# Kernel optimization log

Measured on AMD Instinct MI355X. Metric: run time of the kernel, lower is better.

## Reference

```python
import jax, jax.numpy as jnp
import numpy as np

M = 8      # window size
S = 4      # shift size
NH = 3     # num heads
EPS = 1e-5


def _rel_pos_index(m):
    coords = np.stack(np.meshgrid(np.arange(m), np.arange(m), indexing='ij')).reshape(2, -1)
    rel = (coords[:, :, None] - coords[:, None, :]).transpose(1, 2, 0)
    rel[:, :, 0] += m - 1
    rel[:, :, 1] += m - 1
    rel[:, :, 0] *= 2 * m - 1
    return rel.sum(-1)  # [m^2, m^2]


def _attn_mask(Hs, Ws, m, s):
    img = np.zeros((Hs, Ws))
    cnt = 0
    for hsl in (slice(0, -m), slice(-m, -s), slice(-s, None)):
        for wsl in (slice(0, -m), slice(-m, -s), slice(-s, None)):
            img[hsl, wsl] = cnt
            cnt += 1
    mw = img.reshape(Hs // m, m, Ws // m, m).transpose(0, 2, 1, 3).reshape(-1, m * m)
    d = mw[:, None, :] - mw[:, :, None]
    return np.where(d != 0, -100.0, 0.0).astype(np.float32)  # [nW, N, N]


def _ln(x, w, b):
    mu = jnp.mean(x, -1, keepdims=True)
    var = jnp.mean(jnp.square(x - mu), -1, keepdims=True)
    return (x - mu) * jax.lax.rsqrt(var + EPS) * w + b


def setup_inputs() -> dict:
    key = jax.random.key(0)
    ks = jax.random.split(key, 8)
    B, Hs, Ws, C = 16, 128, 128, 96
    MLPH = 4 * C
    inp = {
        'x': jax.random.normal(ks[0], (B, Hs * Ws, C), jnp.float32),
        'norm1_w': jnp.ones((C,), jnp.float32),
        'norm1_b': jnp.zeros((C,), jnp.float32),
        'qkv_w': jax.random.normal(ks[1], (C, 3 * C), jnp.float32) * 0.02,
        'qkv_b': jnp.zeros((3 * C,), jnp.float32),
        'rpb_table': jax.random.normal(ks[2], ((2 * M - 1) ** 2, NH), jnp.float32) * 0.02,
        'proj_w': jax.random.normal(ks[3], (C, C), jnp.float32) * 0.02,
        'proj_b': jnp.zeros((C,), jnp.float32),
        'norm2_w': jnp.ones((C,), jnp.float32),
        'norm2_b': jnp.zeros((C,), jnp.float32),
        'mlp_w1': jax.random.normal(ks[4], (C, MLPH), jnp.float32) * 0.02,
        'mlp_b1': jnp.zeros((MLPH,), jnp.float32),
        'mlp_w2': jax.random.normal(ks[5], (MLPH, C), jnp.float32) * 0.02,
        'mlp_b2': jnp.zeros((C,), jnp.float32),
        'H': Hs,
        'W': Ws,
    }
    return inp


def reference(x, norm1_w, norm1_b, qkv_w, qkv_b, rpb_table, proj_w, proj_b,
              norm2_w, norm2_b, mlp_w1, mlp_b1, mlp_w2, mlp_b2, H, W):
    B, L, C = x.shape
    N = M * M
    HD = C // NH
    scale = HD ** -0.5
    nW = (H // M) * (W // M)

    rpi = jnp.asarray(_rel_pos_index(M))                    # [N, N]
    mask = jnp.asarray(_attn_mask(H, W, M, S))              # [nW, N, N]

    shortcut = x
    h = _ln(x, norm1_w, norm1_b).reshape(B, H, W, C)
    h = jnp.roll(h, (-S, -S), axis=(1, 2))
    # window partition -> [B, nW, N, C]
    h = h.reshape(B, H // M, M, W // M, M, C).transpose(0, 1, 3, 2, 4, 5)
    h = h.reshape(B, nW, N, C)

    qkv = (h @ qkv_w + qkv_b).reshape(B, nW, N, 3, NH, HD)
    q, k, v = qkv[..., 0, :, :], qkv[..., 1, :, :], qkv[..., 2, :, :]  # [B,nW,N,NH,HD]
    attn = jnp.einsum('bwnhd,bwmhd->bwhnm', q, k) * scale              # [B,nW,NH,N,N]
    rp_bias = rpb_table[rpi].transpose(2, 0, 1)                        # [NH,N,N]
    attn = attn + rp_bias[None, None] + mask[None, :, None]
    attn = jax.nn.softmax(attn, axis=-1)
    out = jnp.einsum('bwhnm,bwmhd->bwnhd', attn, v).reshape(B, nW, N, C)
    out = out @ proj_w + proj_b

    # window reverse -> [B, H, W, C]
    out = out.reshape(B, H // M, W // M, M, M, C).transpose(0, 1, 3, 2, 4, 5)
    out = out.reshape(B, H, W, C)
    out = jnp.roll(out, (S, S), axis=(1, 2)).reshape(B, L, C)

    x1 = shortcut + out
    h2 = _ln(x1, norm2_w, norm2_b)
    h2 = jax.nn.gelu(h2 @ mlp_w1 + mlp_b1, approximate=False) @ mlp_w2 + mlp_b2
    return x1 + h2
```

## Files before the change

kernel.cpp:

```cpp
#include <hip/hip_runtime.h>
#include <hip/hip_bf16.h>

typedef __hip_bfloat16 hbf16;
typedef __bf16 bf16_t;
typedef __bf16 bf16x8 __attribute__((ext_vector_type(8)));
typedef float  f32x4  __attribute__((ext_vector_type(4)));

__device__ __forceinline__ float b2f(hbf16 v) { return __bfloat162float(v); }

__device__ __forceinline__ float ldx(const void* p, size_t i, bool f32) {
    return f32 ? ((const float*)p)[i] : b2f(((const hbf16*)p)[i]);
}

constexpr int Hh  = 128, Ww = 128, Cc = 96;
constexpr int MM  = 8, SS = 4, NHh = 3, C3 = 288;
constexpr int MLPH = 384;
constexpr int NWH = Hh / MM;
constexpr int NW  = NWH * NWH;
constexpr float SCALE = 0.17677669529663687f;
constexpr float EPSf  = 1e-5f;

constexpr int WQKV_ELEMS = C3 * Cc;
constexpr int WP_ELEMS   = Cc * Cc;
constexpr int W1_ELEMS   = MLPH * Cc;
constexpr int W2_ELEMS   = Cc * MLPH;
constexpr int W_TOTAL    = WQKV_ELEMS + WP_ELEMS + W1_ELEMS + W2_ELEMS;

constexpr int OFF_HA  = 0;
constexpr int OFF_QO  = 6144;
constexpr int OFF_KA  = 12288;
constexpr int OFF_VT  = 18432;
constexpr int OFF_HID = 12288;
constexpr int SMEM_E  = 24576;

__global__ void prep_w(const void* __restrict__ qkvw, const void* __restrict__ pw,
                       const void* __restrict__ w1,   const void* __restrict__ w2,
                       const void* __restrict__ n1w,  bf16_t* __restrict__ ws)
{
    const bool f32 = (((const unsigned*)n1w)[0] == 0x3F800000u);
    int i = blockIdx.x * 256 + threadIdx.x;
    if (i < WQKV_ELEMS) {
        int j = i / Cc, k = i - j * Cc;
        ws[i] = (bf16_t)ldx(qkvw, (size_t)k * C3 + j, f32);
    } else if (i < WQKV_ELEMS + WP_ELEMS) {
        int t = i - WQKV_ELEMS;
        int j = t / Cc, k = t - j * Cc;
        ws[i] = (bf16_t)ldx(pw, (size_t)k * Cc + j, f32);
    } else if (i < WQKV_ELEMS + WP_ELEMS + W1_ELEMS) {
        int t = i - WQKV_ELEMS - WP_ELEMS;
        int j = t / Cc, k = t - j * Cc;
        ws[i] = (bf16_t)ldx(w1, (size_t)k * MLPH + j, f32);
    } else if (i < W_TOTAL) {
        int t = i - WQKV_ELEMS - WP_ELEMS - W1_ELEMS;
        int n = t / MLPH, k = t - n * MLPH;
        ws[i] = (bf16_t)ldx(w2, (size_t)k * Cc + n, f32);
    }
}

__global__ __launch_bounds__(256, 3)
void swin_fused(const void* __restrict__ x,
                const void* __restrict__ n1w, const void* __restrict__ n1b,
                const void* __restrict__ qkvb, const void* __restrict__ rpb,
                const void* __restrict__ pb,
                const void* __restrict__ n2w, const void* __restrict__ n2b,
                const void* __restrict__ b1,  const void* __restrict__ b2,
                const bf16_t* __restrict__ wq_t, const bf16_t* __restrict__ wp_t,
                const bf16_t* __restrict__ w1_t, const bf16_t* __restrict__ w2_t,
                float* __restrict__ out)
{
    __shared__ __align__(16) bf16_t sm[SMEM_E];
    const bool f32 = (((const unsigned*)n1w)[0] == 0x3F800000u);

    const int tid  = threadIdx.x;
    const int lane = tid & 63;
    const int wv   = tid >> 6;
    const int c16  = lane & 15;
    const int quad = lane >> 4;
    const int b    = blockIdx.x / NW;
    const int w    = blockIdx.x % NW;
    const int wi   = w / NWH, wj = w % NWH;

    {
        const int t = tid >> 2, q = tid & 3;
        const int ri = wi * MM + (t >> 3), rj = wj * MM + (t & 7);
        const int gi = (ri + SS) & (Hh - 1), gj = (rj + SS) & (Ww - 1);
        const size_t base = ((size_t)((b * Hh + gi) * Ww + gj)) * Cc + q * 24;
        float v[24]; float s = 0.f, s2 = 0.f;
        if (f32) {
            const float* xf = (const float*)x + base;
            #pragma unroll
            for (int i = 0; i < 6; ++i) {
                float4 t4 = *(const float4*)(xf + i * 4);
                v[i*4+0] = t4.x; v[i*4+1] = t4.y; v[i*4+2] = t4.z; v[i*4+3] = t4.w;
            }
        } else {
            #pragma unroll
            for (int i = 0; i < 24; ++i) v[i] = b2f(((const hbf16*)x)[base + i]);
        }
        #pragma unroll
        for (int i = 0; i < 24; ++i) { s += v[i]; s2 += v[i] * v[i]; }
        s  += __shfl_xor(s, 1);  s  += __shfl_xor(s, 2);
        s2 += __shfl_xor(s2, 1); s2 += __shfl_xor(s2, 2);
        const float mu = s / Cc, var = s2 / Cc - mu * mu, rstd = rsqrtf(var + EPSf);
        #pragma unroll
        for (int ch = 0; ch < 3; ++ch) {
            bf16x8 pk;
            #pragma unroll
            for (int i = 0; i < 8; ++i) {
                int cidx = q * 24 + ch * 8 + i;
                pk[i] = (bf16_t)((v[ch * 8 + i] - mu) * rstd * ldx(n1w, cidx, f32) + ldx(n1b, cidx, f32));
            }
            *(bf16x8*)&sm[OFF_HA + ((q * 3 + ch) * 64 + t) * 8] = pk;
        }
    }

    {
        bf16x8 ha[3];
        #pragma unroll
        for (int ks = 0; ks < 3; ++ks)
            ha[ks] = *(const bf16x8*)&sm[OFF_HA + ((ks * 4 + quad) * 64 + wv * 16 + c16) * 8];
        for (int nt = 0; nt < 18; ++nt) {
            const int j = nt * 16 + c16;
            const bf16_t* wrow = wq_t + (size_t)j * Cc + quad * 8;
            bf16x8 b0 = *(const bf16x8*)(wrow);
            bf16x8 b1v = *(const bf16x8*)(wrow + 32);
            bf16x8 b2v = *(const bf16x8*)(wrow + 64);
            f32x4 acc = {0.f, 0.f, 0.f, 0.f};
            acc = __builtin_amdgcn_mfma_f32_16x16x32_bf16(ha[0], b0, acc, 0, 0, 0);
            acc = __builtin_amdgcn_mfma_f32_16x16x32_bf16(ha[1], b1v, acc, 0, 0, 0);
            acc = __builtin_amdgcn_mfma_f32_16x16x32_bf16(ha[2], b2v, acc, 0, 0, 0);
            const float bias = ldx(qkvb, j, f32);
            #pragma unroll
            for (int r = 0; r < 4; ++r) {
                const int m = wv * 16 + quad * 4 + r;
                const bf16_t vb = (bf16_t)(acc[r] + bias);
                if (j < 96) {
                    int hd = j >> 5, d = j & 31;
                    sm[OFF_QO + ((hd * 4 + (d >> 3)) * 64 + m) * 8 + (d & 7)] = vb;
                } else if (j < 192) {
                    int jj = j - 96; int hd = jj >> 5, d = jj & 31;
                    sm[OFF_KA + ((hd * 4 + (d >> 3)) * 64 + m) * 8 + (d & 7)] = vb;
                } else {
                    int jj = j - 192; int hd = jj >> 5, d = jj & 31;
                    sm[OFF_VT + ((hd * 8 + (m >> 3)) * 32 + d) * 8 + (m & 7)] = vb;
                }
            }
        }
    }
    __syncthreads();

    int regq[4];
    #pragma unroll
    for (int r = 0; r < 4; ++r) {
        int qt = wv * 16 + quad * 4 + r;
        int rq = wi * MM + (qt >> 3), cq = wj * MM + (qt & 7);
        regq[r] = (rq < Hh - MM ? 0 : (rq < Hh - SS ? 1 : 2)) * 3
                + (cq < Ww - MM ? 0 : (cq < Ww - SS ? 1 : 2));
    }

    for (int hd = 0; hd < NHh; ++hd) {
        bf16x8 qa = *(const bf16x8*)&sm[OFF_QO + ((hd * 4 + quad) * 64 + wv * 16 + c16) * 8];
        f32x4 sacc[4];
        #pragma unroll
        for (int nt = 0; nt < 4; ++nt) {
            bf16x8 kb = *(const bf16x8*)&sm[OFF_KA + ((hd * 4 + quad) * 64 + nt * 16 + c16) * 8];
            f32x4 z = {0.f, 0.f, 0.f, 0.f};
            sacc[nt] = __builtin_amdgcn_mfma_f32_16x16x32_bf16(qa, kb, z, 0, 0, 0);
        }
        #pragma unroll
        for (int nt = 0; nt < 4; ++nt) {
            const int kt = nt * 16 + c16;
            const int ki = kt >> 3, kj = kt & 7;
            const int rk = wi * MM + ki, ck = wj * MM + kj;
            const int regk = (rk < Hh - MM ? 0 : (rk < Hh - SS ? 1 : 2)) * 3
                           + (ck < Ww - MM ? 0 : (ck < Ww - SS ? 1 : 2));
            #pragma unroll
            for (int r = 0; r < 4; ++r) {
                const int qt = wv * 16 + quad * 4 + r;
                const int qi = qt >> 3, qj = qt & 7;
                const int rpi = (qi - ki + 7) * 15 + (qj - kj + 7);
                float sv = sacc[nt][r] * SCALE + ldx(rpb, (size_t)rpi * NHh + hd, f32);
                if (regq[r] != regk) sv -= 100.0f;
                sacc[nt][r] = sv;
            }
        }
        float inv[4];
        #pragma unroll
        for (int r = 0; r < 4; ++r) {
            float mx = fmaxf(fmaxf(sacc[0][r], sacc[1][r]), fmaxf(sacc[2][r], sacc[3][r]));
            mx = fmaxf(mx, __shfl_xor(mx, 1)); mx = fmaxf(mx, __shfl_xor(mx, 2));
            mx = fmaxf(mx, __shfl_xor(mx, 4)); mx = fmaxf(mx, __shfl_xor(mx, 8));
            float s = 0.f;
            #pragma unroll
            for (int nt = 0; nt < 4; ++nt) { sacc[nt][r] = __expf(sacc[nt][r] - mx); s += sacc[nt][r]; }
            s += __shfl_xor(s, 1); s += __shfl_xor(s, 2);
            s += __shfl_xor(s, 4); s += __shfl_xor(s, 8);
            inv[r] = 1.0f / s;
        }
        #pragma unroll
        for (int nt = 0; nt < 4; ++nt) {
            const int kt = nt * 16 + c16;
            #pragma unroll
            for (int r = 0; r < 4; ++r) {
                const int qt = wv * 16 + quad * 4 + r;
                sm[OFF_HA + ((kt >> 3) * 64 + qt) * 8 + (kt & 7)] = (bf16_t)(sacc[nt][r] * inv[r]);
            }
        }
        #pragma unroll
        for (int nt2 = 0; nt2 < 2; ++nt2) {
            f32x4 acc = {0.f, 0.f, 0.f, 0.f};
            #pragma unroll
            for (int ks = 0; ks < 2; ++ks) {
                bf16x8 pa = *(const bf16x8*)&sm[OFF_HA + ((ks * 4 + quad) * 64 + wv * 16 + c16) * 8];
                bf16x8 vb = *(const bf16x8*)&sm[OFF_VT + ((hd * 8 + ks * 4 + quad) * 32 + nt2 * 16 + c16) * 8];
                acc = __builtin_amdgcn_mfma_f32_16x16x32_bf16(pa, vb, acc, 0, 0, 0);
            }
            const int chan = hd * 32 + nt2 * 16 + c16;
            #pragma unroll
            for (int r = 0; r < 4; ++r) {
                const int m = wv * 16 + quad * 4 + r;
                sm[OFF_QO + ((chan >> 3) * 64 + m) * 8 + (chan & 7)] = (bf16_t)acc[r];
            }
        }
    }

    int gbase[4];
    #pragma unroll
    for (int r = 0; r < 4; ++r) {
        const int m = wv * 16 + quad * 4 + r;
        const int ri = wi * MM + (m >> 3), rj = wj * MM + (m & 7);
        const int gi = (ri + SS) & (Hh - 1), gj = (rj + SS) & (Ww - 1);
        gbase[r] = ((b * Hh + gi) * Ww + gj) * Cc;
    }

    float x1r[24];
    {
        bf16x8 oa[3];
        #pragma unroll
        for (int ks = 0; ks < 3; ++ks)
            oa[ks] = *(const bf16x8*)&sm[OFF_QO + ((ks * 4 + quad) * 64 + wv * 16 + c16) * 8];
        #pragma unroll
        for (int nt = 0; nt < 6; ++nt) {
            const int n = nt * 16 + c16;
            const bf16_t* wrow = wp_t + (size_t)n * Cc + quad * 8;
            f32x4 acc = {0.f, 0.f, 0.f, 0.f};
            acc = __builtin_amdgcn_mfma_f32_16x16x32_bf16(oa[0], *(const bf16x8*)(wrow),      acc, 0, 0, 0);
            acc = __builtin_amdgcn_mfma_f32_16x16x32_bf16(oa[1], *(const bf16x8*)(wrow + 32), acc, 0, 0, 0);
            acc = __builtin_amdgcn_mfma_f32_16x16x32_bf16(oa[2], *(const bf16x8*)(wrow + 64), acc, 0, 0, 0);
            const float bias = ldx(pb, n, f32);
            #pragma unroll
            for (int r = 0; r < 4; ++r)
                x1r[nt * 4 + r] = ldx(x, (size_t)(gbase[r] + n), f32) + acc[r] + bias;
        }
    }

    float mu_[4], rs_[4];
    #pragma unroll
    for (int r = 0; r < 4; ++r) {
        float s = 0.f, s2 = 0.f;
        #pragma unroll
        for (int nt = 0; nt < 6; ++nt) { float v = x1r[nt * 4 + r]; s += v; s2 += v * v; }
        s  += __shfl_xor(s, 1);  s  += __shfl_xor(s, 2);  s  += __shfl_xor(s, 4);  s  += __shfl_xor(s, 8);
        s2 += __shfl_xor(s2, 1); s2 += __shfl_xor(s2, 2); s2 += __shfl_xor(s2, 4); s2 += __shfl_xor(s2, 8);
        float mu = s / Cc, var = s2 / Cc - mu * mu;
        mu_[r] = mu; rs_[r] = rsqrtf(var + EPSf);
    }
    #pragma unroll
    for (int nt = 0; nt < 6; ++nt) {
        const int c = nt * 16 + c16;
        const float wc = ldx(n2w, c, f32), bc = ldx(n2b, c, f32);
        #pragma unroll
        for (int r = 0; r < 4; ++r) {
            const int m = wv * 16 + quad * 4 + r;
            sm[OFF_QO + ((c >> 3) * 64 + m) * 8 + (c & 7)] =
                (bf16_t)((x1r[nt * 4 + r] - mu_[r]) * rs_[r] * wc + bc);
        }
    }
    __syncthreads();

    {
        bf16x8 h2a[3];
        #pragma unroll
        for (int ks = 0; ks < 3; ++ks)
            h2a[ks] = *(const bf16x8*)&sm[OFF_QO + ((ks * 4 + quad) * 64 + wv * 16 + c16) * 8];

        f32x4 acc2[6];
        #pragma unroll
        for (int nt2 = 0; nt2 < 6; ++nt2) acc2[nt2] = {0.f, 0.f, 0.f, 0.f};

        #pragma unroll
        for (int ck = 0; ck < 2; ++ck) {
            for (int nt = 0; nt < 12; ++nt) {
                const int jl = nt * 16 + c16;
                const int j  = ck * 192 + jl;
                const bf16_t* wrow = w1_t + (size_t)j * Cc + quad * 8;
                f32x4 acc = {0.f, 0.f, 0.f, 0.f};
                acc = __builtin_amdgcn_mfma_f32_16x16x32_bf16(h2a[0], *(const bf16x8*)(wrow),      acc, 0, 0, 0);
                acc = __builtin_amdgcn_mfma_f32_16x16x32_bf16(h2a[1], *(const bf16x8*)(wrow + 32), acc, 0, 0, 0);
                acc = __builtin_amdgcn_mfma_f32_16x16x32_bf16(h2a[2], *(const bf16x8*)(wrow + 64), acc, 0, 0, 0);
                const float bj = ldx(b1, j, f32);
                #pragma unroll
                for (int r = 0; r < 4; ++r) {
                    float a = acc[r] + bj;
                    float y = 1.5957691216f * a * (1.0f + 0.044715f * a * a);
                    float g = a / (1.0f + __expf(-y));
                    const int m = wv * 16 + quad * 4 + r;
                    sm[OFF_HID + ((jl >> 3) * 64 + m) * 8 + (jl & 7)] = (bf16_t)g;
                }
            }
            bf16x8 ha2[6];
            #pragma unroll
            for (int ks = 0; ks < 6; ++ks)
                ha2[ks] = *(const bf16x8*)&sm[OFF_HID + ((ks * 4 + quad) * 64 + wv * 16 + c16) * 8];
            #pragma unroll
            for (int nt2 = 0; nt2 < 6; ++nt2) {
                const int n = nt2 * 16 + c16;
                const bf16_t* wrow = w2_t + (size_t)n * MLPH + ck * 192 + quad * 8;
                #pragma unroll
                for (int ks = 0; ks < 6; ++ks)
                    acc2[nt2] = __builtin_amdgcn_mfma_f32_16x16x32_bf16(ha2[ks], *(const bf16x8*)(wrow + ks * 32), acc2[nt2], 0, 0, 0);
            }
        }

        #pragma unroll
        for (int nt2 = 0; nt2 < 6; ++nt2) {
            const int n = nt2 * 16 + c16;
            const float bn = ldx(b2, n, f32);
            #pragma unroll
            for (int r = 0; r < 4; ++r)
                out[gbase[r] + n] = x1r[nt2 * 4 + r] + acc2[nt2][r] + bn;
        }
    }
}

extern "C" void kernel_launch(void* const* d_in, const int* in_sizes, int n_in,
                              void* d_out, int out_size, void* d_ws, size_t ws_size,
                              hipStream_t stream)
{
    const void* x    = d_in[0];
    const void* n1w  = d_in[1];
    const void* n1b  = d_in[2];
    const void* qkvw = d_in[3];
    const void* qkvb = d_in[4];
    const void* rpb  = d_in[5];
    const void* pw   = d_in[6];
    const void* pb   = d_in[7];
    const void* n2w  = d_in[8];
    const void* n2b  = d_in[9];
    const void* w1   = d_in[10];
    const void* b1   = d_in[11];
    const void* w2   = d_in[12];
    const void* b2   = d_in[13];

    const int B = in_sizes[0] / (Hh * Ww * Cc);
    float* out = (float*)d_out;
    bf16_t* wq_t = (bf16_t*)d_ws;
    bf16_t* wp_t = wq_t + WQKV_ELEMS;
    bf16_t* w1_t = wp_t + WP_ELEMS;
    bf16_t* w2_t = w1_t + W1_ELEMS;

    prep_w<<<(W_TOTAL + 255) / 256, 256, 0, stream>>>(qkvw, pw, w1, w2, n1w, wq_t);

    swin_fused<<<B * NW, 256, 0, stream>>>(x, n1w, n1b, qkvb, rpb, pb,
                                           n2w, n2b, b1, b2,
                                           wq_t, wp_t, w1_t, w2_t, out);
}
```

Baseline: 533.4 us.

## Compute transposed attention scores to keep softmax probabilities in registers

```diff
diff --git a/kernel.cpp b/kernel.cpp
--- a/kernel.cpp
+++ b/kernel.cpp
@@ -3,6 +3,7 @@
 
 typedef __hip_bfloat16 hbf16;
 typedef __bf16 bf16_t;
+typedef __bf16 bf16x4 __attribute__((ext_vector_type(4)));
 typedef __bf16 bf16x8 __attribute__((ext_vector_type(8)));
 typedef float  f32x4  __attribute__((ext_vector_type(4)));
 
@@ -26,12 +27,11 @@
 constexpr int W2_ELEMS   = Cc * MLPH;
 constexpr int W_TOTAL    = WQKV_ELEMS + WP_ELEMS + W1_ELEMS + W2_ELEMS;
 
-constexpr int OFF_HA  = 0;
-constexpr int OFF_QO  = 6144;
-constexpr int OFF_KA  = 12288;
-constexpr int OFF_VT  = 18432;
-constexpr int OFF_HID = 12288;
-constexpr int SMEM_E  = 24576;
+constexpr int OFF_A   = 0;
+constexpr int OFF_KA  = 6144;
+constexpr int OFF_VT  = 12288;
+constexpr int OFF_HID = 6144;
+constexpr int SMEM_E  = 18432;
 
 __global__ void prep_w(const void* __restrict__ qkvw, const void* __restrict__ pw,
                        const void* __restrict__ w1,   const void* __restrict__ w2,
@@ -57,7 +57,7 @@
     }
 }
 
-__global__ __launch_bounds__(256, 3)
+__global__ __launch_bounds__(256, 4)
 void swin_fused(const void* __restrict__ x,
                 const void* __restrict__ n1w, const void* __restrict__ n1b,
                 const void* __restrict__ qkvb, const void* __restrict__ rpb,
@@ -110,7 +110,7 @@
                 int cidx = q * 24 + ch * 8 + i;
                 pk[i] = (bf16_t)((v[ch * 8 + i] - mu) * rstd * ldx(n1w, cidx, f32) + ldx(n1b, cidx, f32));
             }
-            *(bf16x8*)&sm[OFF_HA + ((q * 3 + ch) * 64 + t) * 8] = pk;
+            *(bf16x8*)&sm[OFF_A + ((q * 3 + ch) * 64 + t) * 8] = pk;
         }
     }
 
@@ -118,7 +118,7 @@
         bf16x8 ha[3];
         #pragma unroll
         for (int ks = 0; ks < 3; ++ks)
-            ha[ks] = *(const bf16x8*)&sm[OFF_HA + ((ks * 4 + quad) * 64 + wv * 16 + c16) * 8];
+            ha[ks] = *(const bf16x8*)&sm[OFF_A + ((ks * 4 + quad) * 64 + wv * 16 + c16) * 8];
         for (int nt = 0; nt < 18; ++nt) {
             const int j = nt * 16 + c16;
             const bf16_t* wrow = wq_t + (size_t)j * Cc + quad * 8;
@@ -136,7 +136,7 @@
                 const bf16_t vb = (bf16_t)(acc[r] + bias);
                 if (j < 96) {
                     int hd = j >> 5, d = j & 31;
-                    sm[OFF_QO + ((hd * 4 + (d >> 3)) * 64 + m) * 8 + (d & 7)] = vb;
+                    sm[OFF_A + ((hd * 4 + (d >> 3)) * 64 + m) * 8 + (d & 7)] = vb;
                 } else if (j < 192) {
                     int jj = j - 96; int hd = jj >> 5, d = jj & 31;
                     sm[OFF_KA + ((hd * 4 + (d >> 3)) * 64 + m) * 8 + (d & 7)] = vb;
@@ -149,77 +149,93 @@
     }
     __syncthreads();
 
-    int regq[4];
-    #pragma unroll
-    for (int r = 0; r < 4; ++r) {
-        int qt = wv * 16 + quad * 4 + r;
-        int rq = wi * MM + (qt >> 3), cq = wj * MM + (qt & 7);
-        regq[r] = (rq < Hh - MM ? 0 : (rq < Hh - SS ? 1 : 2)) * 3
-                + (cq < Ww - MM ? 0 : (cq < Ww - SS ? 1 : 2));
-    }
-
-    for (int hd = 0; hd < NHh; ++hd) {
-        bf16x8 qa = *(const bf16x8*)&sm[OFF_QO + ((hd * 4 + quad) * 64 + wv * 16 + c16) * 8];
-        f32x4 sacc[4];
-        #pragma unroll
-        for (int nt = 0; nt < 4; ++nt) {
-            bf16x8 kb = *(const bf16x8*)&sm[OFF_KA + ((hd * 4 + quad) * 64 + nt * 16 + c16) * 8];
-            f32x4 z = {0.f, 0.f, 0.f, 0.f};
-            sacc[nt] = __builtin_amdgcn_mfma_f32_16x16x32_bf16(qa, kb, z, 0, 0, 0);
-        }
-        #pragma unroll
-        for (int nt = 0; nt < 4; ++nt) {
-            const int kt = nt * 16 + c16;
-            const int ki = kt >> 3, kj = kt & 7;
-            const int rk = wi * MM + ki, ck = wj * MM + kj;
-            const int regk = (rk < Hh - MM ? 0 : (rk < Hh - SS ? 1 : 2)) * 3
-                           + (ck < Ww - MM ? 0 : (ck < Ww - SS ? 1 : 2));
+    const int qt_tok = wv * 16 + c16;
+    const int qi = qt_tok >> 3, qj = qt_tok & 7;
+    {
+        const int rq = wi * MM + qi, cq = wj * MM + qj;
+        const int regq = (rq < Hh - MM ? 0 : (rq < Hh - SS ? 1 : 2)) * 3
+                       + (cq < Ww - MM ? 0 : (cq < Ww - SS ? 1 : 2));
+        int   rpi16[16];
+        float pen16[16];
+        #pragma unroll
+        for (int nt = 0; nt < 4; ++nt)
             #pragma unroll
             for (int r = 0; r < 4; ++r) {
-                const int qt = wv * 16 + quad * 4 + r;
-                const int qi = qt >> 3, qj = qt & 7;
-                const int rpi = (qi - ki + 7) * 15 + (qj - kj + 7);
-                float sv = sacc[nt][r] * SCALE + ldx(rpb, (size_t)rpi * NHh + hd, f32);
-                if (regq[r] != regk) sv -= 100.0f;
-                sacc[nt][r] = sv;
-            }
-        }
-        float inv[4];
-        #pragma unroll
-        for (int r = 0; r < 4; ++r) {
-            float mx = fmaxf(fmaxf(sacc[0][r], sacc[1][r]), fmaxf(sacc[2][r], sacc[3][r]));
-            mx = fmaxf(mx, __shfl_xor(mx, 1)); mx = fmaxf(mx, __shfl_xor(mx, 2));
-            mx = fmaxf(mx, __shfl_xor(mx, 4)); mx = fmaxf(mx, __shfl_xor(mx, 8));
+                const int k = nt * 16 + quad * 4 + r;
+                const int ki = k >> 3, kj = k & 7;
+                const int rk = wi * MM + ki, ck = wj * MM + kj;
+                const int regk = (rk < Hh - MM ? 0 : (rk < Hh - SS ? 1 : 2)) * 3
+                               + (ck < Ww - MM ? 0 : (ck < Ww - SS ? 1 : 2));
+                rpi16[nt * 4 + r] = ((qi - ki + 7) * 15 + (qj - kj + 7)) * NHh;
+                pen16[nt * 4 + r] = (regq != regk) ? -100.0f : 0.0f;
+            }
+
+        for (int hd = 0; hd < NHh; ++hd) {
+            bf16x8 qa = *(const bf16x8*)&sm[OFF_A + ((hd * 4 + quad) * 64 + qt_tok) * 8];
+            f32x4 sacc[4];
+            #pragma unroll
+            for (int nt = 0; nt < 4; ++nt) {
+                bf16x8 kb = *(const bf16x8*)&sm[OFF_KA + ((hd * 4 + quad) * 64 + nt * 16 + c16) * 8];
+                f32x4 z = {0.f, 0.f, 0.f, 0.f};
+                sacc[nt] = __builtin_amdgcn_mfma_f32_16x16x32_bf16(kb, qa, z, 0, 0, 0);
+            }
+            #pragma unroll
+            for (int nt = 0; nt < 4; ++nt)
+                #pragma unroll
+                for (int r = 0; r < 4; ++r)
+                    sacc[nt][r] = sacc[nt][r] * SCALE
+                                + ldx(rpb, (size_t)(rpi16[nt * 4 + r] + hd), f32)
+                                + pen16[nt * 4 + r];
+            f32x4 m4 = sacc[0];
+            #pragma unroll
+            for (int nt = 1; nt < 4; ++nt)
+                #pragma unroll
+                for (int r = 0; r < 4; ++r) m4[r] = fmaxf(m4[r], sacc[nt][r]);
+            float mx = fmaxf(fmaxf(m4[0], m4[1]), fmaxf(m4[2], m4[3]));
+            mx = fmaxf(mx, __shfl_xor(mx, 16));
+            mx = fmaxf(mx, __shfl_xor(mx, 32));
             float s = 0.f;
             #pragma unroll
-            for (int nt = 0; nt < 4; ++nt) { sacc[nt][r] = __expf(sacc[nt][r] - mx); s += sacc[nt][r]; }
-            s += __shfl_xor(s, 1); s += __shfl_xor(s, 2);
-            s += __shfl_xor(s, 4); s += __shfl_xor(s, 8);
-            inv[r] = 1.0f / s;
-        }
-        #pragma unroll
-        for (int nt = 0; nt < 4; ++nt) {
-            const int kt = nt * 16 + c16;
+            for (int nt = 0; nt < 4; ++nt)
+                #pragma unroll
+                for (int r = 0; r < 4; ++r) {
+                    float e = __expf(sacc[nt][r] - mx);
+                    sacc[nt][r] = e; s += e;
+                }
+            s += __shfl_xor(s, 16);
+            s += __shfl_xor(s, 32);
+            const float inv = 1.0f / s;
+            bf16x8 pb01, pb23;
             #pragma unroll
             for (int r = 0; r < 4; ++r) {
-                const int qt = wv * 16 + quad * 4 + r;
-                sm[OFF_HA + ((kt >> 3) * 64 + qt) * 8 + (kt & 7)] = (bf16_t)(sacc[nt][r] * inv[r]);
-            }
-        }
-        #pragma unroll
-        for (int nt2 = 0; nt2 < 2; ++nt2) {
-            f32x4 acc = {0.f, 0.f, 0.f, 0.f};
-            #pragma unroll
-            for (int ks = 0; ks < 2; ++ks) {
-                bf16x8 pa = *(const bf16x8*)&sm[OFF_HA + ((ks * 4 + quad) * 64 + wv * 16 + c16) * 8];
-                bf16x8 vb = *(const bf16x8*)&sm[OFF_VT + ((hd * 8 + ks * 4 + quad) * 32 + nt2 * 16 + c16) * 8];
-                acc = __builtin_amdgcn_mfma_f32_16x16x32_bf16(pa, vb, acc, 0, 0, 0);
-            }
-            const int chan = hd * 32 + nt2 * 16 + c16;
-            #pragma unroll
-            for (int r = 0; r < 4; ++r) {
-                const int m = wv * 16 + quad * 4 + r;
-                sm[OFF_QO + ((chan >> 3) * 64 + m) * 8 + (chan & 7)] = (bf16_t)acc[r];
+                pb01[r]     = (bf16_t)(sacc[0][r] * inv);
+                pb01[4 + r] = (bf16_t)(sacc[1][r] * inv);
+                pb23[r]     = (bf16_t)(sacc[2][r] * inv);
+                pb23[4 + r] = (bf16_t)(sacc[3][r] * inv);
+            }
+            const int g2 = quad >> 1, o2 = (quad & 1) * 4;
+            #pragma unroll
+            for (int ct = 0; ct < 2; ++ct) {
+                const int d = ct * 16 + c16;
+                const int vb0 = OFF_VT + ((hd * 8 + g2) * 32 + d) * 8 + o2;
+                bf16x4 v0 = *(const bf16x4*)&sm[vb0];
+                bf16x4 v1 = *(const bf16x4*)&sm[vb0 + 512];
+                bf16x4 v2 = *(const bf16x4*)&sm[vb0 + 1024];
+                bf16x4 v3 = *(const bf16x4*)&sm[vb0 + 1536];
+                bf16x8 va01, va23;
+                #pragma unroll
+                for (int i = 0; i < 4; ++i) {
+                    va01[i] = v0[i]; va01[4 + i] = v1[i];
+                    va23[i] = v2[i]; va23[4 + i] = v3[i];
+                }
+                f32x4 acc = {0.f, 0.f, 0.f, 0.f};
+                acc = __builtin_amdgcn_mfma_f32_16x16x32_bf16(va01, pb01, acc, 0, 0, 0);
+                acc = __builtin_amdgcn_mfma_f32_16x16x32_bf16(va23, pb23, acc, 0, 0, 0);
+                bf16x4 ov;
+                #pragma unroll
+                for (int r = 0; r < 4; ++r) ov[r] = (bf16_t)acc[r];
+                const int cg = hd * 4 + ct * 2 + g2;
+                *(bf16x4*)&sm[OFF_A + (cg * 64 + qt_tok) * 8 + o2] = ov;
             }
         }
     }
@@ -238,7 +254,7 @@
         bf16x8 oa[3];
         #pragma unroll
         for (int ks = 0; ks < 3; ++ks)
-            oa[ks] = *(const bf16x8*)&sm[OFF_QO + ((ks * 4 + quad) * 64 + wv * 16 + c16) * 8];
+            oa[ks] = *(const bf16x8*)&sm[OFF_A + ((ks * 4 + quad) * 64 + wv * 16 + c16) * 8];
         #pragma unroll
         for (int nt = 0; nt < 6; ++nt) {
             const int n = nt * 16 + c16;
@@ -272,7 +288,7 @@
         #pragma unroll
         for (int r = 0; r < 4; ++r) {
             const int m = wv * 16 + quad * 4 + r;
-            sm[OFF_QO + ((c >> 3) * 64 + m) * 8 + (c & 7)] =
+            sm[OFF_A + ((c >> 3) * 64 + m) * 8 + (c & 7)] =
                 (bf16_t)((x1r[nt * 4 + r] - mu_[r]) * rs_[r] * wc + bc);
         }
     }
@@ -282,7 +298,7 @@
         bf16x8 h2a[3];
         #pragma unroll
         for (int ks = 0; ks < 3; ++ks)
-            h2a[ks] = *(const bf16x8*)&sm[OFF_QO + ((ks * 4 + quad) * 64 + wv * 16 + c16) * 8];
+            h2a[ks] = *(const bf16x8*)&sm[OFF_A + ((ks * 4 + quad) * 64 + wv * 16 + c16) * 8];
 
         f32x4 acc2[6];
         #pragma unroll
```

Measured after the change: 525.6 us. Within noise of the previous version (-1.4%).
